# Performance work log

Measured on AMD Instinct MI355X. Metric: run time of the kernel, lower is better.

Reference implementation:

```python
import jax, jax.numpy as jnp
import numpy as np

N = 50000          # nodes
E = 1600000        # edges (avg degree 32)
IN = 9             # raw node feature dim
D = 128            # hidden / out channels
G = 64             # number of graphs in batch
EPS = 1e-5         # LayerNorm eps (torch default)


def _layernorm(h, gamma, beta):
    m = jnp.mean(h, axis=-1, keepdims=True)
    v = jnp.mean((h - m) ** 2, axis=-1, keepdims=True)
    return (h - m) * jax.lax.rsqrt(v + EPS) * gamma + beta


def _sage_conv(h, src, dst, W, b):
    # scatter-mean of neighbor features onto dst, then linear on concat(self, mean)
    nsum = jax.ops.segment_sum(h[src], dst, num_segments=N)            # (N, d)
    cnt = jax.ops.segment_sum(jnp.ones((src.shape[0], 1), h.dtype), dst, num_segments=N)
    nmean = nsum / jnp.maximum(cnt, 1.0)
    return jnp.concatenate([h, nmean], axis=-1) @ W + b               # (N, out)


def setup_inputs() -> dict:
    key = jax.random.key(0)
    ks = jax.random.split(key, 16)
    x = jax.random.normal(ks[0], (N, IN), dtype=jnp.float32)
    edge_index = jax.random.randint(ks[1], (2, E), 0, N, dtype=jnp.int64)
    batch = jnp.sort(jax.random.randint(ks[2], (N,), 0, G, dtype=jnp.int64))

    def lin(k, fin, fout):
        kw, kb = jax.random.split(k)
        s = 1.0 / np.sqrt(fin)
        W = jax.random.uniform(kw, (fin, fout), jnp.float32, -s, s)
        b = jax.random.uniform(kb, (fout,), jnp.float32, -s, s)
        return W, b

    W_emb, b_emb = lin(ks[3], IN, D)
    Wc1, bc1 = lin(ks[4], 2 * D, D)
    Wc2, bc2 = lin(ks[5], 2 * D, D)
    Wc3, bc3 = lin(ks[6], 2 * D, D)
    ones = jnp.ones((D,), jnp.float32)
    zeros = jnp.zeros((D,), jnp.float32)
    return {
        "x": x, "edge_index": edge_index, "batch": batch,
        "W_emb": W_emb, "b_emb": b_emb, "g0": ones, "bt0": zeros,
        "Wc1": Wc1, "bc1": bc1, "g1": ones, "bt1": zeros,
        "Wc2": Wc2, "bc2": bc2, "g2": ones, "bt2": zeros,
        "Wc3": Wc3, "bc3": bc3, "g3": ones, "bt3": zeros,
    }


def reference(x, edge_index, batch, W_emb, b_emb, g0, bt0,
              Wc1, bc1, g1, bt1, Wc2, bc2, g2, bt2, Wc3, bc3, g3, bt3):
    src, dst = edge_index[0], edge_index[1]
    # node embedder: Linear -> LayerNorm -> ReLU
    h = jax.nn.relu(_layernorm(x @ W_emb + b_emb, g0, bt0))
    # 3 SAGE layers (dropout is identity in eval mode)
    h = jax.nn.relu(_layernorm(_sage_conv(h, src, dst, Wc1, bc1), g1, bt1))
    h = jax.nn.relu(_layernorm(_sage_conv(h, src, dst, Wc2, bc2), g2, bt2))
    node_embed = jax.nn.relu(_layernorm(_sage_conv(h, src, dst, Wc3, bc3), g3, bt3))
    # graph pooling: mean + max over nodes per graph
    gsum = jax.ops.segment_sum(node_embed, batch, num_segments=G)
    gcnt = jax.ops.segment_sum(jnp.ones((N, 1), node_embed.dtype), batch, num_segments=G)
    h_mean = gsum / jnp.maximum(gcnt, 1.0)
    h_max = jax.ops.segment_max(node_embed, batch, num_segments=G)  # -inf identity matches torch init
    graph_embed = jnp.concatenate([h_mean, h_max], axis=-1)
    return node_embed, graph_embed
```

## Files before the change

### kernel.cpp

```cpp
#include <hip/hip_runtime.h>
#include <hip/hip_bf16.h>
#include <math.h>

#define NN 50000
#define NNP 50048
#define NE 1600000
#define FIN 9
#define DD 128
#define NG 64
#define PSEG 16
#define LN_EPS 1e-5f

#define NB 196
#define BSHIFT 8
#define CH 8192
#define MAXBE 12288
#define MAXPB 20480
#define EMB0 387

typedef __attribute__((ext_vector_type(8))) short bf16x8;
typedef __attribute__((ext_vector_type(4))) float f32x4;
typedef __attribute__((ext_vector_type(2))) float f32x2;

static __device__ __forceinline__ unsigned short f2b(float f) {
  __hip_bfloat16 h = __float2bfloat16(f);
  return __builtin_bit_cast(unsigned short, h);
}
static __device__ __forceinline__ unsigned char f2e4m3(float f) {
  int r = __builtin_amdgcn_cvt_pk_fp8_f32(f, f, 0, false);
  return (unsigned char)(r & 0xFF);
}

__global__ __launch_bounds__(256) void k_prep(const float* __restrict__ Wc1,
                                              const float* __restrict__ Wc2,
                                              const float* __restrict__ Wc3,
                                              unsigned short* __restrict__ Wt1,
                                              unsigned short* __restrict__ Wt2,
                                              unsigned short* __restrict__ Wt3,
                                              int* __restrict__ bcur,
                                              const int* __restrict__ batch,
                                              int* __restrict__ gstart,
                                              unsigned short* __restrict__ hba,
                                              unsigned short* __restrict__ hbb,
                                              unsigned char* __restrict__ h8,
                                              unsigned short* __restrict__ hmb,
                                              float* __restrict__ gout,
                                              const float* __restrict__ x,
                                              const float* __restrict__ W,
                                              const float* __restrict__ b,
                                              const float* __restrict__ gamma,
                                              const float* __restrict__ beta) {
  const int bid = blockIdx.x;
  const int t = threadIdx.x;
  if (bid < 384) {
    const float* Wc = (bid < 128) ? Wc1 : (bid < 256) ? Wc2 : Wc3;
    unsigned short* Wt = (bid < 128) ? Wt1 : (bid < 256) ? Wt2 : Wt3;
    int idx = (bid & 127) * 256 + t;
    int k = idx >> 7;
    int n = idx & 127;
    Wt[n * 256 + k] = f2b(Wc[k * DD + n]);
    return;
  }
  if (bid == 384) {
    if (t < NB) bcur[t] = t * MAXBE;
    if (t >= 128 && t <= 128 + NG) {
      int g = t - 128;
      int lo = 0, hi = NN;
      while (lo < hi) {
        int mid = (lo + hi) >> 1;
        if (batch[mid] < g) lo = mid + 1; else hi = mid;
      }
      gstart[g] = lo;
    }
    return;
  }
  if (bid == 385) {
    unsigned int* pa = reinterpret_cast<unsigned int*>(hba + (size_t)NN * DD);
    unsigned int* pb = reinterpret_cast<unsigned int*>(hbb + (size_t)NN * DD);
    unsigned int* pm = reinterpret_cast<unsigned int*>(hmb + (size_t)NN * DD);
    unsigned int* p8 = reinterpret_cast<unsigned int*>(h8 + (size_t)NN * DD);
    const int n2 = (NNP - NN) * DD / 2;
    for (int i = t; i < n2; i += 256) { pa[i] = 0; pb[i] = 0; pm[i] = 0; }
    for (int i = t; i < (NNP - NN) * DD / 4; i += 256) p8[i] = 0;
    return;
  }
  if (bid == 386) {
    for (int i = t; i < NG * 256; i += 256) gout[i] = 0.f;
    return;
  }
  const int wid = t >> 6;
  const int lane = t & 63;
  const int node = (bid - EMB0) * 4 + wid;
  if (node >= NN) return;
  float xr[FIN];
#pragma unroll
  for (int k = 0; k < FIN; ++k) xr[k] = x[node * FIN + k];
  const int c0 = lane, c1 = lane + 64;
  float a0 = b[c0], a1 = b[c1];
#pragma unroll
  for (int k = 0; k < FIN; ++k) {
    a0 += xr[k] * W[k * DD + c0];
    a1 += xr[k] * W[k * DD + c1];
  }
  float s = a0 + a1;
#pragma unroll
  for (int m = 1; m < 64; m <<= 1) s += __shfl_xor(s, m, 64);
  float mean = s * (1.f / DD);
  float d0 = a0 - mean, d1 = a1 - mean;
  float v = d0 * d0 + d1 * d1;
#pragma unroll
  for (int m = 1; m < 64; m <<= 1) v += __shfl_xor(v, m, 64);
  float r = rsqrtf(v * (1.f / DD) + LN_EPS);
  float o0 = fmaxf(d0 * r * gamma[c0] + beta[c0], 0.f);
  float o1 = fmaxf(d1 * r * gamma[c1] + beta[c1], 0.f);
  hba[(size_t)node * DD + c0] = f2b(o0);
  hba[(size_t)node * DD + c1] = f2b(o1);
  h8[(size_t)node * DD + c0] = f2e4m3(o0);
  h8[(size_t)node * DD + c1] = f2e4m3(o1);
}

__global__ __launch_bounds__(512) void k_bscatter(const int* __restrict__ src,
                                                  const int* __restrict__ dst,
                                                  int* __restrict__ bcur,
                                                  unsigned int* __restrict__ bents) {
  __shared__ int lh[NB], lbase[NB], gbase[NB], lcnt[NB];
  __shared__ int stmp[256];
  __shared__ unsigned int sbuf[CH];
  const int t = threadIdx.x;
  const int e0 = blockIdx.x * CH;
  const int n = min(CH, NE - e0);

  for (int i = t; i < NB; i += 512) { lh[i] = 0; lcnt[i] = 0; }
  __syncthreads();

  unsigned int ent[16];
  int eb[16];
#pragma unroll
  for (int k = 0; k < 16; ++k) {
    int i = k * 512 + t;
    if (i < n) {
      int s = src[e0 + i], d = dst[e0 + i];
      ent[k] = ((unsigned)d << 16) | (unsigned)s;
      eb[k] = d >> BSHIFT;
      atomicAdd(&lh[eb[k]], 1);
    } else {
      eb[k] = -1;
    }
  }
  __syncthreads();
  if (t < 256) stmp[t] = (t < NB) ? lh[t] : 0;
  __syncthreads();
  for (int off = 1; off < 256; off <<= 1) {
    int v = 0;
    if (t < 256 && t >= off) v = stmp[t - off];
    __syncthreads();
    if (t < 256) stmp[t] += v;
    __syncthreads();
  }
  if (t < NB) lbase[t] = (t == 0) ? 0 : stmp[t - 1];
  __syncthreads();
  if (t < NB && lh[t] > 0) gbase[t] = atomicAdd(&bcur[t], lh[t]);
  __syncthreads();
#pragma unroll
  for (int k = 0; k < 16; ++k) {
    if (eb[k] >= 0) {
      int r = atomicAdd(&lcnt[eb[k]], 1);
      sbuf[lbase[eb[k]] + r] = ent[k];
    }
  }
  __syncthreads();
  for (int i = t; i < n; i += 512) {
    unsigned int e = sbuf[i];
    int b = e >> 24;
    int pos = gbase[b] + (i - lbase[b]);
    if (pos < (b + 1) * MAXBE) bents[pos] = e;
  }
}

__global__ __launch_bounds__(512) void k_sort(const unsigned int* __restrict__ bents,
                                              const int* __restrict__ bcur,
                                              int* __restrict__ prowptr,
                                              int* __restrict__ degv,
                                              unsigned short* __restrict__ csr16) {
  __shared__ int lh[256], lsc[256], plsc[256], lc2[256];
  const int b = blockIdx.x, t = threadIdx.x;
  const int base = b * MAXBE;
  const int nb = min(bcur[b] - base, MAXBE);
  const int pbase = b * MAXPB;

  if (t < 256) { lh[t] = 0; lc2[t] = 0; }
  __syncthreads();
  for (int i = t; i < nb; i += 512)
    atomicAdd(&lh[(bents[base + i] >> 16) & 255], 1);
  __syncthreads();
  if (t < 256) { lsc[t] = lh[t]; plsc[t] = (lh[t] + 31) & ~31; }
  __syncthreads();
  for (int off = 1; off < 256; off <<= 1) {
    int v = 0, pv = 0;
    if (t < 256 && t >= off) { v = lsc[t - off]; pv = plsc[t - off]; }
    __syncthreads();
    if (t < 256) { lsc[t] += v; plsc[t] += pv; }
    __syncthreads();
  }
  int ex = 0, pex = 0;
  if (t < 256) { ex = (t == 0) ? 0 : lsc[t - 1]; pex = (t == 0) ? 0 : plsc[t - 1]; }
  __syncthreads();
  if (t < 256) {
    lsc[t] = ex;
    plsc[t] = pex;
    int gnode = b * 256 + t;
    if (gnode < NN) { prowptr[gnode] = pbase + pex; degv[gnode] = lh[t]; }
  }
  __syncthreads();
  for (int i = t; i < nb; i += 512) {
    unsigned int e = bents[base + i];
    int dl = (e >> 16) & 255;
    int r = atomicAdd(&lc2[dl], 1);
    csr16[pbase + plsc[dl] + r] = (unsigned short)(e & 0xFFFF);
  }
  __syncthreads();
  if (t < 256) {
    int d = lh[t];
    int pd = (d + 31) & ~31;
    int o = pbase + plsc[t];
    for (int k = d; k < pd; ++k) csr16[o + k] = (unsigned short)NN;
  }
}

__global__ __launch_bounds__(256) void k_aggr(const unsigned char* __restrict__ h8,
                                              const int* __restrict__ prowptr,
                                              const int* __restrict__ degv,
                                              const unsigned short* __restrict__ csr16,
                                              unsigned short* __restrict__ hmb) {
  const int wid = __builtin_amdgcn_readfirstlane(threadIdx.x >> 6);
  const int l = threadIdx.x & 63;
  const int lh = l & 31;
  const int hi = l >> 5;
  const int node = blockIdx.x * 4 + wid;
  const int pbeg = __builtin_amdgcn_readfirstlane(prowptr[node]);
  const int deg = __builtin_amdgcn_readfirstlane(degv[node]);
  const int nch = (deg + 31) >> 5;
  const unsigned int* __restrict__ cp =
      reinterpret_cast<const unsigned int*>(csr16 + pbeg);
  float a0 = 0.f, a1 = 0.f, a2 = 0.f, a3 = 0.f;
  for (int c = 0; c < nch; ++c) {
#pragma unroll
    for (int q = 0; q < 16; ++q) {
      unsigned int pair = cp[c * 16 + q];
      int row = hi ? (int)(pair >> 16) : (int)(pair & 0xFFFFu);
      const unsigned int* rp =
          reinterpret_cast<const unsigned int*>(h8 + (size_t)row * DD);
      unsigned int u = rp[lh];
      f32x2 dlo = __builtin_amdgcn_cvt_pk_f32_fp8((int)u, false);
      f32x2 dhi = __builtin_amdgcn_cvt_pk_f32_fp8((int)u, true);
      a0 += dlo.x; a1 += dlo.y; a2 += dhi.x; a3 += dhi.y;
    }
  }
  a0 += __shfl_xor(a0, 32, 64);
  a1 += __shfl_xor(a1, 32, 64);
  a2 += __shfl_xor(a2, 32, 64);
  a3 += __shfl_xor(a3, 32, 64);
  if (hi == 0) {
    float inv = 1.f / (float)max(deg, 1);
    ushort4 o;
    o.x = f2b(a0 * inv); o.y = f2b(a1 * inv);
    o.z = f2b(a2 * inv); o.w = f2b(a3 * inv);
    reinterpret_cast<ushort4*>(hmb + (size_t)node * DD)[lh] = o;
  }
}

template <int OUT_BF16>
__global__ __launch_bounds__(512, 4) void k_lin_mfma(const unsigned short* __restrict__ hb,
                                                     const unsigned short* __restrict__ hmb,
                                                     const unsigned short* __restrict__ Wt,
                                                     const float* __restrict__ bias,
                                                     const float* __restrict__ gamma,
                                                     const float* __restrict__ beta,
                                                     void* __restrict__ outv,
                                                     unsigned char* __restrict__ h8out) {
  __shared__ unsigned short wlds[128 * 256];
  __shared__ float sred[4][16][2][2];
  const int tid = threadIdx.x;
  const int w = tid >> 6;
  const int l = tid & 63;
  const int g = w & 3;
  const int hh = w >> 2;
  const int c16 = l & 15;
  const int kg = l >> 4;
  const int node = blockIdx.x * 64 + g * 16 + c16;

#pragma unroll
  for (int it = 0; it < 8; ++it) {
    int idx = it * 512 + tid;
    int r = idx >> 5;
    int gr = idx & 31;
    uint4 v = *reinterpret_cast<const uint4*>(Wt + (size_t)r * 256 + gr * 8);
    int gs = gr ^ (r & 7);
    *reinterpret_cast<uint4*>(wlds + (size_t)r * 256 + gs * 8) = v;
  }

  const unsigned short* brow_self = hb + (size_t)node * DD + kg * 8;
  const unsigned short* brow_mean = hmb + (size_t)node * DD + kg * 8;
  bf16x8 bfr[8];
#pragma unroll
  for (int kc = 0; kc < 4; ++kc)
    bfr[kc] = *reinterpret_cast<const bf16x8*>(brow_self + kc * 32);
#pragma unroll
  for (int kc = 0; kc < 4; ++kc)
    bfr[4 + kc] = *reinterpret_cast<const bf16x8*>(brow_mean + kc * 32);

  __syncthreads();

  f32x4 acc[4];
#pragma unroll
  for (int t2 = 0; t2 < 4; ++t2) acc[t2] = (f32x4){0.f, 0.f, 0.f, 0.f};

#pragma unroll
  for (int t2 = 0; t2 < 4; ++t2) {
    const int row = (hh * 4 + t2) * 16 + c16;
    const unsigned short* wr = wlds + (size_t)row * 256;
    const int sw = c16 & 7;
#pragma unroll
    for (int kc = 0; kc < 8; ++kc) {
      bf16x8 a = *reinterpret_cast<const bf16x8*>(wr + ((kc * 4 + kg) ^ sw) * 8);
      acc[t2] = __builtin_amdgcn_mfma_f32_16x16x32_bf16(a, bfr[kc], acc[t2], 0, 0, 0);
    }
  }

#pragma unroll
  for (int t2 = 0; t2 < 4; ++t2) {
    float4 bv = reinterpret_cast<const float4*>(bias)[(hh * 4 + t2) * 4 + kg];
    acc[t2][0] += bv.x; acc[t2][1] += bv.y; acc[t2][2] += bv.z; acc[t2][3] += bv.w;
  }

  float s = 0.f, q = 0.f;
#pragma unroll
  for (int t2 = 0; t2 < 4; ++t2)
#pragma unroll
    for (int i = 0; i < 4; ++i) { float v = acc[t2][i]; s += v; q += v * v; }
#pragma unroll
  for (int m = 16; m < 64; m <<= 1) {
    s += __shfl_xor(s, m, 64);
    q += __shfl_xor(q, m, 64);
  }
  if (kg == 0) { sred[g][c16][hh][0] = s; sred[g][c16][hh][1] = q; }
  __syncthreads();
  float st = sred[g][c16][0][0] + sred[g][c16][1][0];
  float qt = sred[g][c16][0][1] + sred[g][c16][1][1];
  float mean = st * (1.f / DD);
  float var = fmaxf(qt * (1.f / DD) - mean * mean, 0.f);
  float r = rsqrtf(var + LN_EPS);

  if (node < NN) {
#pragma unroll
    for (int t2 = 0; t2 < 4; ++t2) {
      int cbase = (hh * 4 + t2) * 16 + kg * 4;
      float4 gv = reinterpret_cast<const float4*>(gamma)[cbase >> 2];
      float4 btv = reinterpret_cast<const float4*>(beta)[cbase >> 2];
      float v0 = fmaxf((acc[t2][0] - mean) * r * gv.x + btv.x, 0.f);
      float v1 = fmaxf((acc[t2][1] - mean) * r * gv.y + btv.y, 0.f);
      float v2 = fmaxf((acc[t2][2] - mean) * r * gv.z + btv.z, 0.f);
      float v3 = fmaxf((acc[t2][3] - mean) * r * gv.w + btv.w, 0.f);
      if (OUT_BF16) {
        ushort4 ob;
        ob.x = f2b(v0); ob.y = f2b(v1); ob.z = f2b(v2); ob.w = f2b(v3);
        *reinterpret_cast<ushort4*>((unsigned short*)outv + (size_t)node * DD + cbase) = ob;
        int p8 = __builtin_amdgcn_cvt_pk_fp8_f32(v0, v1, 0, false);
        p8 = __builtin_amdgcn_cvt_pk_fp8_f32(v2, v3, p8, true);
        *reinterpret_cast<unsigned int*>(h8out + (size_t)node * DD + cbase) = (unsigned int)p8;
      } else {
        float4 of = make_float4(v0, v1, v2, v3);
        *reinterpret_cast<float4*>((float*)outv + (size_t)node * DD + cbase) = of;
      }
    }
  }
}

__global__ __launch_bounds__(128) void k_pool(const float* __restrict__ ne,
                                              const int* __restrict__ gstart,
                                              float* __restrict__ gout) {
  const int g = blockIdx.x / PSEG;
  const int sg = blockIdx.x % PSEG;
  const int c = threadIdx.x;
  const int beg = gstart[g], end = gstart[g + 1];
  const int len = end - beg;
  const int per = (len + PSEG - 1) / PSEG;
  const int n0 = beg + sg * per;
  const int n1 = min(n0 + per, end);
  float s = 0.f, mx = 0.f;
  for (int n = n0; n < n1; ++n) {
    float v = ne[(size_t)n * DD + c];
    s += v;
    mx = fmaxf(mx, v);
  }
  atomicAdd(&gout[(size_t)g * 256 + c], s / (float)max(len, 1));
  atomicMax(reinterpret_cast<int*>(&gout[(size_t)g * 256 + 128 + c]), __float_as_int(mx));
}

static inline size_t align_up(size_t v, size_t a) { return (v + a - 1) & ~(a - 1); }

extern "C" void kernel_launch(void* const* d_in, const int* in_sizes, int n_in,
                              void* d_out, int out_size, void* d_ws, size_t ws_size,
                              hipStream_t stream) {
  const float* x     = (const float*)d_in[0];
  const int*   ei    = (const int*)d_in[1];
  const int*   batch = (const int*)d_in[2];
  const float* W_emb = (const float*)d_in[3];
  const float* b_emb = (const float*)d_in[4];
  const float* g0    = (const float*)d_in[5];
  const float* bt0   = (const float*)d_in[6];
  const float* Wc1   = (const float*)d_in[7];
  const float* bc1   = (const float*)d_in[8];
  const float* g1    = (const float*)d_in[9];
  const float* bt1   = (const float*)d_in[10];
  const float* Wc2   = (const float*)d_in[11];
  const float* bc2   = (const float*)d_in[12];
  const float* g2    = (const float*)d_in[13];
  const float* bt2   = (const float*)d_in[14];
  const float* Wc3   = (const float*)d_in[15];
  const float* bc3   = (const float*)d_in[16];
  const float* g3    = (const float*)d_in[17];
  const float* bt3   = (const float*)d_in[18];

  const int* src = ei;
  const int* dst = ei + NE;

  float* out_node  = (float*)d_out;
  float* out_graph = (float*)d_out + (size_t)NN * DD;

  char* p = (char*)d_ws;
  auto alloc = [&](size_t bytes) { char* r = p; p += align_up(bytes, 256); return r; };
  int*            prowptr = (int*)alloc((size_t)NN * sizeof(int));
  int*            degv    = (int*)alloc((size_t)NN * sizeof(int));
  int*            bcur    = (int*)alloc(NB * sizeof(int));
  int*            gstart  = (int*)alloc((NG + 1) * sizeof(int));
  unsigned int*   bents   = (unsigned int*)alloc((size_t)NB * MAXBE * 4);
  unsigned short* csr16   = (unsigned short*)alloc((size_t)NB * MAXPB * 2);
  unsigned short* hba     = (unsigned short*)alloc((size_t)NNP * DD * 2);
  unsigned short* hbb     = (unsigned short*)alloc((size_t)NNP * DD * 2);
  unsigned char*  h8      = (unsigned char*)alloc((size_t)NNP * DD);
  unsigned short* hmb     = (unsigned short*)alloc((size_t)NNP * DD * 2);
  unsigned short* Wt1     = (unsigned short*)alloc(128 * 256 * 2);
  unsigned short* Wt2     = (unsigned short*)alloc(128 * 256 * 2);
  unsigned short* Wt3     = (unsigned short*)alloc(128 * 256 * 2);

  k_prep<<<EMB0 + NN / 4, 256, 0, stream>>>(Wc1, Wc2, Wc3, Wt1, Wt2, Wt3, bcur, batch,
                                            gstart, hba, hbb, h8, hmb, out_graph,
                                            x, W_emb, b_emb, g0, bt0);
  k_bscatter<<<(NE + CH - 1) / CH, 512, 0, stream>>>(src, dst, bcur, bents);
  k_sort<<<NB, 512, 0, stream>>>(bents, bcur, prowptr, degv, csr16);

  const int LIN_GRID = NNP / 64;
  const int AGGR_GRID = NN / 4;
  k_aggr<<<AGGR_GRID, 256, 0, stream>>>(h8, prowptr, degv, csr16, hmb);
  k_lin_mfma<1><<<LIN_GRID, 512, 0, stream>>>(hba, hmb, Wt1, bc1, g1, bt1, hbb, h8);
  k_aggr<<<AGGR_GRID, 256, 0, stream>>>(h8, prowptr, degv, csr16, hmb);
  k_lin_mfma<1><<<LIN_GRID, 512, 0, stream>>>(hbb, hmb, Wt2, bc2, g2, bt2, hba, h8);
  k_aggr<<<AGGR_GRID, 256, 0, stream>>>(h8, prowptr, degv, csr16, hmb);
  k_lin_mfma<0><<<LIN_GRID, 512, 0, stream>>>(hba, hmb, Wt3, bc3, g3, bt3, out_node, h8);

  k_pool<<<NG * PSEG, 128, 0, stream>>>(out_node, gstart, out_graph);
}
```

Before: 206.6 us.

## Split fp8 feature table into two 64-column planes for aggregation

Stores the fp8 node-feature table as two column-half planes (64 bytes per node each) and doubles the aggregation grid so each block handles one half-plane. Each wave now gathers four neighbor rows at a time with 16 lanes per 64-byte row, instead of two rows with 32 lanes. The aim is a smaller gather working set per pass, for better L2/MALL hit rates, and more concurrent rows in flight. In exchange every CSR index is read twice, and the writers in the embedding and linear kernels must produce the planar layout.

```diff
diff --git a/kernel.cpp b/kernel.cpp
--- a/kernel.cpp
+++ b/kernel.cpp
@@ -30,6 +30,7 @@
   int r = __builtin_amdgcn_cvt_pk_fp8_f32(f, f, 0, false);
   return (unsigned char)(r & 0xFF);
 }
+
 
 __global__ __launch_bounds__(256) void k_prep(const float* __restrict__ Wc1,
                                               const float* __restrict__ Wc2,
@@ -78,10 +79,11 @@
     unsigned int* pa = reinterpret_cast<unsigned int*>(hba + (size_t)NN * DD);
     unsigned int* pb = reinterpret_cast<unsigned int*>(hbb + (size_t)NN * DD);
     unsigned int* pm = reinterpret_cast<unsigned int*>(hmb + (size_t)NN * DD);
-    unsigned int* p8 = reinterpret_cast<unsigned int*>(h8 + (size_t)NN * DD);
+    unsigned int* p8a = reinterpret_cast<unsigned int*>(h8 + (size_t)NN * 64);
+    unsigned int* p8b = reinterpret_cast<unsigned int*>(h8 + (size_t)NNP * 64 + (size_t)NN * 64);
     const int n2 = (NNP - NN) * DD / 2;
     for (int i = t; i < n2; i += 256) { pa[i] = 0; pb[i] = 0; pm[i] = 0; }
-    for (int i = t; i < (NNP - NN) * DD / 4; i += 256) p8[i] = 0;
+    for (int i = t; i < (NNP - NN) * 64 / 4; i += 256) { p8a[i] = 0; p8b[i] = 0; }
     return;
   }
   if (bid == 386) {
@@ -115,8 +117,8 @@
   float o1 = fmaxf(d1 * r * gamma[c1] + beta[c1], 0.f);
   hba[(size_t)node * DD + c0] = f2b(o0);
   hba[(size_t)node * DD + c1] = f2b(o1);
-  h8[(size_t)node * DD + c0] = f2e4m3(o0);
-  h8[(size_t)node * DD + c1] = f2e4m3(o1);
+  h8[(size_t)node * 64 + lane] = f2e4m3(o0);
+  h8[(size_t)NNP * 64 + (size_t)node * 64 + lane] = f2e4m3(o1);
 }
 
 __global__ __launch_bounds__(512) void k_bscatter(const int* __restrict__ src,
@@ -232,40 +234,46 @@
                                               const int* __restrict__ degv,
                                               const unsigned short* __restrict__ csr16,
                                               unsigned short* __restrict__ hmb) {
+  const int bid = blockIdx.x;
+  const int r8 = bid & 7;
+  const int half = r8 >> 2;
+  const int nq = (bid >> 3) * 4 + (r8 & 3);
   const int wid = __builtin_amdgcn_readfirstlane(threadIdx.x >> 6);
   const int l = threadIdx.x & 63;
-  const int lh = l & 31;
-  const int hi = l >> 5;
-  const int node = blockIdx.x * 4 + wid;
+  const int eq = l >> 4;
+  const int cd = l & 15;
+  const int node = nq * 4 + wid;
   const int pbeg = __builtin_amdgcn_readfirstlane(prowptr[node]);
   const int deg = __builtin_amdgcn_readfirstlane(degv[node]);
   const int nch = (deg + 31) >> 5;
   const unsigned int* __restrict__ cp =
       reinterpret_cast<const unsigned int*>(csr16 + pbeg);
+  const unsigned char* __restrict__ plane = h8 + (size_t)half * NNP * 64;
   float a0 = 0.f, a1 = 0.f, a2 = 0.f, a3 = 0.f;
   for (int c = 0; c < nch; ++c) {
 #pragma unroll
-    for (int q = 0; q < 16; ++q) {
-      unsigned int pair = cp[c * 16 + q];
-      int row = hi ? (int)(pair >> 16) : (int)(pair & 0xFFFFu);
-      const unsigned int* rp =
-          reinterpret_cast<const unsigned int*>(h8 + (size_t)row * DD);
-      unsigned int u = rp[lh];
+    for (int s = 0; s < 8; ++s) {
+      unsigned int pa = cp[c * 16 + 2 * s];
+      unsigned int pb = cp[c * 16 + 2 * s + 1];
+      unsigned int pr = (eq >> 1) ? pb : pa;
+      int row = (eq & 1) ? (int)(pr >> 16) : (int)(pr & 0xFFFFu);
+      unsigned int u =
+          reinterpret_cast<const unsigned int*>(plane + (size_t)row * 64)[cd];
       f32x2 dlo = __builtin_amdgcn_cvt_pk_f32_fp8((int)u, false);
       f32x2 dhi = __builtin_amdgcn_cvt_pk_f32_fp8((int)u, true);
       a0 += dlo.x; a1 += dlo.y; a2 += dhi.x; a3 += dhi.y;
     }
   }
-  a0 += __shfl_xor(a0, 32, 64);
-  a1 += __shfl_xor(a1, 32, 64);
-  a2 += __shfl_xor(a2, 32, 64);
-  a3 += __shfl_xor(a3, 32, 64);
-  if (hi == 0) {
+  a0 += __shfl_xor(a0, 16, 64); a1 += __shfl_xor(a1, 16, 64);
+  a2 += __shfl_xor(a2, 16, 64); a3 += __shfl_xor(a3, 16, 64);
+  a0 += __shfl_xor(a0, 32, 64); a1 += __shfl_xor(a1, 32, 64);
+  a2 += __shfl_xor(a2, 32, 64); a3 += __shfl_xor(a3, 32, 64);
+  if (eq == 0) {
     float inv = 1.f / (float)max(deg, 1);
     ushort4 o;
     o.x = f2b(a0 * inv); o.y = f2b(a1 * inv);
     o.z = f2b(a2 * inv); o.w = f2b(a3 * inv);
-    reinterpret_cast<ushort4*>(hmb + (size_t)node * DD)[lh] = o;
+    reinterpret_cast<ushort4*>(hmb + (size_t)node * DD + half * 64)[cd] = o;
   }
 }
 
@@ -367,7 +375,8 @@
         *reinterpret_cast<ushort4*>((unsigned short*)outv + (size_t)node * DD + cbase) = ob;
         int p8 = __builtin_amdgcn_cvt_pk_fp8_f32(v0, v1, 0, false);
         p8 = __builtin_amdgcn_cvt_pk_fp8_f32(v2, v3, p8, true);
-        *reinterpret_cast<unsigned int*>(h8out + (size_t)node * DD + cbase) = (unsigned int)p8;
+        *reinterpret_cast<unsigned int*>(h8out + (size_t)(cbase >> 6) * NNP * 64 +
+                                         (size_t)node * 64 + (cbase & 63)) = (unsigned int)p8;
       } else {
         float4 of = make_float4(v0, v1, v2, v3);
         *reinterpret_cast<float4*>((float*)outv + (size_t)node * DD + cbase) = of;
@@ -438,7 +447,7 @@
   unsigned short* csr16   = (unsigned short*)alloc((size_t)NB * MAXPB * 2);
   unsigned short* hba     = (unsigned short*)alloc((size_t)NNP * DD * 2);
   unsigned short* hbb     = (unsigned short*)alloc((size_t)NNP * DD * 2);
-  unsigned char*  h8      = (unsigned char*)alloc((size_t)NNP * DD);
+  unsigned char*  h8      = (unsigned char*)alloc((size_t)2 * NNP * 64);
   unsigned short* hmb     = (unsigned short*)alloc((size_t)NNP * DD * 2);
   unsigned short* Wt1     = (unsigned short*)alloc(128 * 256 * 2);
   unsigned short* Wt2     = (unsigned short*)alloc(128 * 256 * 2);
@@ -451,7 +460,7 @@
   k_sort<<<NB, 512, 0, stream>>>(bents, bcur, prowptr, degv, csr16);
 
   const int LIN_GRID = NNP / 64;
-  const int AGGR_GRID = NN / 4;
+  const int AGGR_GRID = (NN / 4) * 2;
   k_aggr<<<AGGR_GRID, 256, 0, stream>>>(h8, prowptr, degv, csr16, hmb);
   k_lin_mfma<1><<<LIN_GRID, 512, 0, stream>>>(hba, hmb, Wt1, bc1, g1, bt1, hbb, h8);
   k_aggr<<<AGGR_GRID, 256, 0, stream>>>(h8, prowptr, degv, csr16, hmb);
```

New measurement: 236.0 us. 1.14x slower.
